# Kernel optimization log

Measured on AMD Instinct MI355X. Metric: run time of the kernel, lower is better.

The kernel has to match this reference:

```python
import jax, jax.numpy as jnp
import numpy as np

B0 = 0.01       # baseline threshold (Yin et al. ALIF)
BETA = 1.8      # adaptation coupling strength
SG_GAMMA = 0.5  # surrogate gradient scale
SG_LENS = 0.5   # surrogate gradient width

@jax.custom_vjp
def spike(v):
    return (v > 0.0).astype(v.dtype)

def _spike_fwd(v):
    return spike(v), v

def _spike_bwd(v, g):
    sg = SG_GAMMA * jnp.exp(-0.5 * (v / SG_LENS) ** 2) / (jnp.sqrt(2.0 * jnp.pi) * SG_LENS)
    return (g * sg,)

spike.defvjp(_spike_fwd, _spike_bwd)

def alif_forward(x, W_h, tau_mem, tau_adp, W_o, tau_out):
    # x: [T, B, I]; W_h: [H, I+H]; W_o: [O, H]
    T, B, _ = x.shape
    H = W_h.shape[0]
    O = W_o.shape[0]
    alpha = jnp.exp(-1.0 / tau_mem)    # [H] membrane decay
    rho = jnp.exp(-1.0 / tau_adp)      # [H] adaptation decay
    alpha_o = jnp.exp(-1.0 / tau_out)  # [O] output leaky-integrator decay
    z0 = jnp.zeros((B, H), x.dtype)
    u0 = jnp.zeros((B, H), x.dtype)
    a0 = jnp.zeros((B, H), x.dtype)
    ou0 = jnp.zeros((B, O), x.dtype)

    def step(carry, x_t):
        z, u, a, ou = carry
        cur = jnp.concatenate([x_t, z], axis=1) @ W_h.T   # [B, H]
        a = rho * a + (1.0 - rho) * z                     # adaptation from previous spike
        theta = B0 + BETA * a                             # adaptive threshold
        u = alpha * u + (1.0 - alpha) * cur - z * theta   # leaky integrate + soft reset
        z = spike(u - theta)                              # heaviside w/ surrogate grad
        ou = alpha_o * ou + (1.0 - alpha_o) * (z @ W_o.T) # LI readout
        return (z, u, a, ou), (ou, jnp.sum(z))

    (zT, uT, aT, ouT), (outputs, spikes) = jax.lax.scan(step, (z0, u0, a0, ou0), x)
    return outputs, (zT, uT, aT, ouT), jnp.sum(spikes)

def setup_inputs() -> dict:
    key = jax.random.key(0)
    ks = jax.random.split(key, 6)
    T, B, I, H, O = 250, 256, 700, 1024, 20
    x = jax.random.normal(ks[0], (T, B, I), jnp.float32)
    W_h = jax.random.normal(ks[1], (H, I + H), jnp.float32) / np.sqrt(I + H).astype(np.float32)
    tau_mem = 20.0 + 5.0 * jax.random.normal(ks[2], (H,), jnp.float32)
    tau_adp = 20.0 + 5.0 * jax.random.normal(ks[3], (H,), jnp.float32)
    W_o = jax.random.normal(ks[4], (O, H), jnp.float32) / np.sqrt(H).astype(np.float32)
    tau_out = 20.0 + 5.0 * jax.random.normal(ks[5], (O,), jnp.float32)
    return {"x": x, "W_h": W_h, "tau_mem": tau_mem, "tau_adp": tau_adp, "W_o": W_o, "tau_out": tau_out}

def reference(x, W_h, tau_mem, tau_adp, W_o, tau_out):
    outputs, (zT, uT, aT, ouT), num_spikes = alif_forward(x, W_h, tau_mem, tau_adp, W_o, tau_out)
    # matches torch forward: (outputs, ((hidden_z, hidden_u, hidden_a), out_u), num_spikes)
    return (outputs, zT, uT, aT, ouT, num_spikes)
```

## Files before the change

### kernel.cpp

```cpp
#include <hip/hip_runtime.h>

#define T_STEPS 250
#define BATCH   256
#define IN_DIM  700
#define HID     1024
#define W_LD    1724
#define OUT_DIM 20
#define KP      704
#define KP4     (KP / 4)
#define NKT     (KP / 32)
#define CHUNK_T 50

typedef __attribute__((ext_vector_type(8))) short     bf16x8;
typedef __attribute__((ext_vector_type(8))) unsigned short u16x8;
typedef __attribute__((ext_vector_type(4))) float     f32x4;
typedef unsigned long long u64;

__device__ inline unsigned short f2bf(float f) {
    unsigned int u = __float_as_uint(f);
    unsigned int r = u + 0x7FFFu + ((u >> 16) & 1u);
    return (unsigned short)(r >> 16);
}

__global__ __launch_bounds__(256)
void trans_whh_bf16(const float* __restrict__ W_h, unsigned short* __restrict__ WhhT) {
    __shared__ float tile[32][33];
    const int bx = blockIdx.x * 32;
    const int by = blockIdx.y * 32;
    const int tx = threadIdx.x, ty = threadIdx.y;
#pragma unroll
    for (int i = 0; i < 32; i += 8)
        tile[ty + i][tx] = W_h[(size_t)(bx + ty + i) * W_LD + IN_DIM + by + tx];
    __syncthreads();
#pragma unroll
    for (int i = 0; i < 32; i += 8)
        WhhT[(size_t)(by + ty + i) * HID + bx + tx] = f2bf(tile[tx][ty + i]);
}

__global__ __launch_bounds__(256)
void trans_wo(const float* __restrict__ Wo, float* __restrict__ WoT) {
    const int h = blockIdx.x * 256 + threadIdx.x;
    if (h >= HID) return;
#pragma unroll
    for (int o = 0; o < OUT_DIM; ++o)
        WoT[(size_t)h * OUT_DIM + o] = Wo[(size_t)o * HID + h];
}

__global__ __launch_bounds__(256)
void pack_x_bf16(const float* __restrict__ x, unsigned short* __restrict__ Xp, int rows) {
    const int total = rows * KP4;
    for (int idx = blockIdx.x * blockDim.x + threadIdx.x; idx < total;
         idx += gridDim.x * blockDim.x) {
        const int r = idx / KP4;
        const int c = idx - r * KP4;
        ushort4 o = make_ushort4(0, 0, 0, 0);
        if (c < IN_DIM / 4) {
            float4 v = *(const float4*)(x + (size_t)r * IN_DIM + c * 4);
            o = make_ushort4(f2bf(v.x), f2bf(v.y), f2bf(v.z), f2bf(v.w));
        }
        ((ushort4*)Xp)[(size_t)r * KP4 + c] = o;
    }
}

__global__ __launch_bounds__(256)
void pack_w_bf16(const float* __restrict__ W_h, unsigned short* __restrict__ Wp) {
    const int total = HID * KP4;
    for (int idx = blockIdx.x * blockDim.x + threadIdx.x; idx < total;
         idx += gridDim.x * blockDim.x) {
        const int r = idx / KP4;
        const int c = idx - r * KP4;
        ushort4 o = make_ushort4(0, 0, 0, 0);
        if (c < IN_DIM / 4) {
            float4 v = *(const float4*)(W_h + (size_t)r * W_LD + c * 4);
            o = make_ushort4(f2bf(v.x), f2bf(v.y), f2bf(v.z), f2bf(v.w));
        }
        ((ushort4*)Wp)[(size_t)r * KP4 + c] = o;
    }
}

__global__ __launch_bounds__(256)
void mfma_gemm(const unsigned short* __restrict__ A,
               const unsigned short* __restrict__ B, float* __restrict__ C) {
    __shared__ unsigned short lA[128 * 32];
    __shared__ unsigned short lB[128 * 32];
    const int tid  = threadIdx.x;
    const int wid  = tid >> 6, lane = tid & 63;
    const int wr   = wid >> 1, wc = wid & 1;
    const size_t bm = (size_t)blockIdx.x * 128;
    const size_t bn = (size_t)blockIdx.y * 128;

    const int srow = tid >> 2;
    const int skq  = (tid & 3) * 8;

    const int wb0 = (srow * 64 + (tid & 3) * 16) ^ ((srow & 7) << 4);
    const int wb1 = ((srow + 64) * 64 + (tid & 3) * 16) ^ ((srow & 7) << 4);

    const unsigned short* pa = A + (bm + srow) * KP + skq;
    const unsigned short* pb = B + (bn + srow) * KP + skq;

    u16x8 ra0, ra1, rb0, rb1;
    auto ldg = [&](int k0) {
        ra0 = *(const u16x8*)(pa + k0);
        ra1 = *(const u16x8*)(pa + (size_t)64 * KP + k0);
        rb0 = *(const u16x8*)(pb + k0);
        rb1 = *(const u16x8*)(pb + (size_t)64 * KP + k0);
    };

    const int arow = wr * 64 + (lane & 15);
    const int brow = wc * 64 + (lane & 15);
    const int fq   = (lane >> 4) * 16;

    f32x4 acc[4][4];
#pragma unroll
    for (int m = 0; m < 4; ++m)
#pragma unroll
        for (int n = 0; n < 4; ++n) acc[m][n] = (f32x4){0.f, 0.f, 0.f, 0.f};

    ldg(0);
    for (int kt = 0; kt < NKT; ++kt) {
        *(u16x8*)((char*)lA + wb0) = ra0;
        *(u16x8*)((char*)lA + wb1) = ra1;
        *(u16x8*)((char*)lB + wb0) = rb0;
        *(u16x8*)((char*)lB + wb1) = rb1;
        __syncthreads();
        if (kt + 1 < NKT) ldg((kt + 1) * 32);
        bf16x8 af[4], bf[4];
#pragma unroll
        for (int m = 0; m < 4; ++m) {
            const int row = arow + m * 16;
            af[m] = *(const bf16x8*)((const char*)lA + ((row * 64 + fq) ^ ((row & 7) << 4)));
        }
#pragma unroll
        for (int n = 0; n < 4; ++n) {
            const int row = brow + n * 16;
            bf[n] = *(const bf16x8*)((const char*)lB + ((row * 64 + fq) ^ ((row & 7) << 4)));
        }
#pragma unroll
        for (int m = 0; m < 4; ++m)
#pragma unroll
            for (int n = 0; n < 4; ++n)
                acc[m][n] = __builtin_amdgcn_mfma_f32_16x16x32_bf16(af[m], bf[n], acc[m][n], 0, 0, 0);
        __syncthreads();
    }
#pragma unroll
    for (int m = 0; m < 4; ++m)
#pragma unroll
        for (int r = 0; r < 4; ++r) {
            float* cp = C + (bm + wr * 64 + m * 16 + (lane >> 4) * 4 + r) * HID
                          + bn + wc * 64 + (lane & 15);
#pragma unroll
            for (int n = 0; n < 4; ++n) cp[n * 16] = acc[m][n][r];
        }
}

#define G_LDIDX(JJ, g)                                                        \
    {                                                                         \
        const int base_ = lo + (g) * 4;                                       \
        JJ[0] = (base_ + 0 < hi) ? (int)lst[base_ + 0] : 1024;                \
        JJ[1] = (base_ + 1 < hi) ? (int)lst[base_ + 1] : 1024;                \
        JJ[2] = (base_ + 2 < hi) ? (int)lst[base_ + 2] : 1024;                \
        JJ[3] = (base_ + 3 < hi) ? (int)lst[base_ + 3] : 1024;                \
    }

#define G_ISSUE(WB, JJ)                                                       \
    {                                                                         \
        _Pragma("unroll")                                                     \
        for (int q_ = 0; q_ < 4; ++q_) {                                      \
            const unsigned int* p_ = Wrow32 + ((size_t)JJ[q_] << 9);          \
            WB[q_ * 2 + 0] = *(const uint4*)p_;                               \
            WB[q_ * 2 + 1] = *(const uint4*)(p_ + 4);                         \
        }                                                                     \
    }

#define G_ACCUM(WB)                                                           \
    {                                                                         \
        _Pragma("unroll")                                                     \
        for (int q_ = 0; q_ < 4; ++q_) {                                      \
            const uint4 w0_ = WB[q_ * 2 + 0];                                 \
            const uint4 w1_ = WB[q_ * 2 + 1];                                 \
            pacc[0][0] += __uint_as_float(w0_.x << 16);                       \
            pacc[0][1] += __uint_as_float(w0_.x & 0xFFFF0000u);               \
            pacc[0][2] += __uint_as_float(w0_.y << 16);                       \
            pacc[0][3] += __uint_as_float(w0_.y & 0xFFFF0000u);               \
            pacc[1][0] += __uint_as_float(w0_.z << 16);                       \
            pacc[1][1] += __uint_as_float(w0_.z & 0xFFFF0000u);               \
            pacc[1][2] += __uint_as_float(w0_.w << 16);                       \
            pacc[1][3] += __uint_as_float(w0_.w & 0xFFFF0000u);               \
            pacc[2][0] += __uint_as_float(w1_.x << 16);                       \
            pacc[2][1] += __uint_as_float(w1_.x & 0xFFFF0000u);               \
            pacc[2][2] += __uint_as_float(w1_.y << 16);                       \
            pacc[2][3] += __uint_as_float(w1_.y & 0xFFFF0000u);               \
            pacc[3][0] += __uint_as_float(w1_.z << 16);                       \
            pacc[3][1] += __uint_as_float(w1_.z & 0xFFFF0000u);               \
            pacc[3][2] += __uint_as_float(w1_.w << 16);                       \
            pacc[3][3] += __uint_as_float(w1_.w & 0xFFFF0000u);               \
        }                                                                     \
    }

__global__ __launch_bounds__(256, 1)
void alif_scan(const float* __restrict__ CUR, const unsigned short* __restrict__ WhhT,
               const float* __restrict__ tau_mem, const float* __restrict__ tau_adp,
               float* __restrict__ zS, float* __restrict__ uS, float* __restrict__ aS,
               float* __restrict__ spkS, unsigned short* __restrict__ masks16,
               int t0, int tc) {
    const int tid  = threadIdx.x;
    const int wv   = tid >> 6;
    const int lane = tid & 63;
    const int b    = blockIdx.x;
    const int h0   = lane * 16;

    __shared__ __align__(16) unsigned short s_idx[4][2][1040];
    __shared__ __align__(16) f32x4 s_part[4][4][64];

    float u[16], a[16], alpha[16], rho[16];
#pragma unroll
    for (int q = 0; q < 4; ++q) {
        f32x4 uu = *(const f32x4*)(uS + (size_t)b * HID + h0 + q * 4);
        f32x4 aa = *(const f32x4*)(aS + (size_t)b * HID + h0 + q * 4);
        f32x4 tm = *(const f32x4*)(tau_mem + h0 + q * 4);
        f32x4 ta = *(const f32x4*)(tau_adp + h0 + q * 4);
#pragma unroll
        for (int k = 0; k < 4; ++k) {
            u[q * 4 + k] = uu[k];  a[q * 4 + k] = aa[k];
            alpha[q * 4 + k] = expf(-1.f / tm[k]);
            rho[q * 4 + k]   = expf(-1.f / ta[k]);
        }
    }
    unsigned int zb = 0;
#pragma unroll
    for (int q = 0; q < 4; ++q) {
        f32x4 zz = *(const f32x4*)(zS + (size_t)b * HID + h0 + q * 4);
#pragma unroll
        for (int k = 0; k < 4; ++k)
            if (zz[k] > 0.5f) zb |= (1u << (q * 4 + k));
    }

    int n;
    {
        const int cnt = __popc(zb);
        int incl = cnt;
#pragma unroll
        for (int d = 1; d < 64; d <<= 1) {
            int v = __shfl_up(incl, d, 64);
            if (lane >= d) incl += v;
        }
        int off = incl - cnt;
        unsigned int tmp = zb;
        while (tmp) {
            const int k = __ffs(tmp) - 1;
            tmp &= tmp - 1;
            s_idx[wv][0][off++] = (unsigned short)(h0 + k);
        }
        n = __shfl(incl, 63, 64);
    }

    const unsigned int* Wrow32 = (const unsigned int*)WhhT + (h0 >> 1);
    float xc[16];
#pragma unroll
    for (int q = 0; q < 4; ++q) {
        f32x4 v = *(const f32x4*)(CUR + (size_t)b * HID + h0 + q * 4);
        xc[q*4+0]=v[0]; xc[q*4+1]=v[1]; xc[q*4+2]=v[2]; xc[q*4+3]=v[3];
    }
    __syncthreads();

    int cur = 0;
    int wspk = 0;
    for (int tt = 0; tt < tc; ++tt) {
        float xn[16];
        {
            const int tn = (tt + 1 < tc) ? tt + 1 : tt;
            const float* p = CUR + ((size_t)tn * BATCH + b) * HID + h0;
#pragma unroll
            for (int q = 0; q < 4; ++q) {
                f32x4 v = *(const f32x4*)(p + q * 4);
                xn[q*4+0]=v[0]; xn[q*4+1]=v[1]; xn[q*4+2]=v[2]; xn[q*4+3]=v[3];
            }
        }

        f32x4 pacc[4];
#pragma unroll
        for (int q = 0; q < 4; ++q) pacc[q] = (f32x4){0.f, 0.f, 0.f, 0.f};

        if (n > 0) {
            const unsigned short* lst = s_idx[wv][cur];
            const int lo = (n * wv) >> 2;
            const int hi = (n * (wv + 1)) >> 2;
            const int m = hi - lo;
            if (m > 0) {
                const int ng = (m + 3) >> 2;
                int  jA[4], jB[4];
                uint4 wA[8], wB[8];
                G_LDIDX(jA, 0);
                G_ISSUE(wA, jA);
                int g = 0;
                while (true) {
                    if (g + 1 < ng) { G_LDIDX(jB, g + 1); G_ISSUE(wB, jB); }
                    G_ACCUM(wA);
                    if (++g >= ng) break;
                    if (g + 1 < ng) { G_LDIDX(jA, g + 1); G_ISSUE(wA, jA); }
                    G_ACCUM(wB);
                    if (++g >= ng) break;
                }
            }
            s_part[wv][0][lane] = pacc[0];
            s_part[wv][1][lane] = pacc[1];
            s_part[wv][2][lane] = pacc[2];
            s_part[wv][3][lane] = pacc[3];
            __syncthreads();
#pragma unroll
            for (int q = 0; q < 4; ++q) {
                f32x4 r0 = s_part[0][q][lane];
                f32x4 r1 = s_part[1][q][lane];
                f32x4 r2 = s_part[2][q][lane];
                f32x4 r3 = s_part[3][q][lane];
                pacc[q] = ((r0 + r1) + r2) + r3;
            }
        }

        unsigned int znb = 0;
#pragma unroll
        for (int k = 0; k < 16; ++k) {
            const float rec = pacc[k >> 2][k & 3];
            const float z   = (zb >> k) & 1 ? 1.f : 0.f;
            const float omr = 1.f - rho[k];
            const float oma = 1.f - alpha[k];
            a[k] = rho[k] * a[k] + omr * z;
            const float th = 0.01f + 1.8f * a[k];
            u[k] = alpha[k] * u[k] + oma * (xc[k] + rec) - z * th;
            if (u[k] - th > 0.f) znb |= (1u << k);
        }
        zb = znb;
        wspk += __popc(zb);
        if (wv == 0)
            masks16[((size_t)(t0 + tt) * BATCH + b) * 64 + lane] = (unsigned short)zb;

        {
            const int cnt = __popc(zb);
            int incl = cnt;
#pragma unroll
            for (int d = 1; d < 64; d <<= 1) {
                int v = __shfl_up(incl, d, 64);
                if (lane >= d) incl += v;
            }
            int off = incl - cnt;
            unsigned int tmp = zb;
            while (tmp) {
                const int k = __ffs(tmp) - 1;
                tmp &= tmp - 1;
                s_idx[wv][cur ^ 1][off++] = (unsigned short)(h0 + k);
            }
            n = __shfl(incl, 63, 64);
        }
#pragma unroll
        for (int k = 0; k < 16; ++k) xc[k] = xn[k];
        __syncthreads();
        cur ^= 1;
    }

    if (wv == 0) {
#pragma unroll
        for (int k = 0; k < 16; ++k) {
            zS[(size_t)b * HID + h0 + k] = (zb >> k) & 1 ? 1.f : 0.f;
            uS[(size_t)b * HID + h0 + k] = u[k];
            aS[(size_t)b * HID + h0 + k] = a[k];
        }
#pragma unroll
        for (int d = 32; d > 0; d >>= 1) wspk += __shfl_down(wspk, d, 64);
        if (lane == 0) atomicAdd(spkS, (float)wspk);
    }
}

__global__ __launch_bounds__(256)
void readout_y(const u64* __restrict__ masks, const float* __restrict__ WoT,
               float* __restrict__ y, int npairs) {
    const int pr   = blockIdx.x * 4 + (threadIdx.x >> 6);
    const int lane = threadIdx.x & 63;
    if (pr >= npairs) return;
    const u64* mp = masks + (size_t)pr * 16;
    float acc = 0.f;
#pragma unroll 4
    for (int w = 0; w < 16; ++w) {
        u64 m = mp[w];
        while (m) {
            const int j = __ffsll((unsigned long long)m) - 1;
            m &= m - 1;
            if (lane < OUT_DIM) acc += WoT[(size_t)(w * 64 + j) * OUT_DIM + lane];
        }
    }
    if (lane < OUT_DIM) y[(size_t)pr * OUT_DIM + lane] = acc;
}

__global__ __launch_bounds__(256)
void ewa_out(const float* __restrict__ y, const float* __restrict__ tau_out,
             float* __restrict__ outputs, float* __restrict__ ouS) {
    const int idx = blockIdx.x * 256 + threadIdx.x;
    if (idx >= BATCH * OUT_DIM) return;
    const int o = idx % OUT_DIM;
    const float ao = expf(-1.f / tau_out[o]);
    float ou = ouS[idx];
    for (int t = 0; t < T_STEPS; ++t) {
        const float v = y[(size_t)t * BATCH * OUT_DIM + idx];
        ou = ao * ou + (1.f - ao) * v;
        outputs[(size_t)t * BATCH * OUT_DIM + idx] = ou;
    }
    ouS[idx] = ou;
}

extern "C" void kernel_launch(void* const* d_in, const int* in_sizes, int n_in,
                              void* d_out, int out_size, void* d_ws, size_t ws_size,
                              hipStream_t stream) {
    (void)in_sizes; (void)n_in; (void)out_size;
    const float* x       = (const float*)d_in[0];
    const float* W_h     = (const float*)d_in[1];
    const float* tau_mem = (const float*)d_in[2];
    const float* tau_adp = (const float*)d_in[3];
    const float* W_o     = (const float*)d_in[4];
    const float* tau_out = (const float*)d_in[5];

    float* out     = (float*)d_out;
    float* outputs = out;
    float* zS  = out + (size_t)T_STEPS * BATCH * OUT_DIM;
    float* uS  = zS + (size_t)BATCH * HID;
    float* aS  = uS + (size_t)BATCH * HID;
    float* ouS = aS + (size_t)BATCH * HID;
    float* spk = ouS + (size_t)BATCH * OUT_DIM;

    char* w = (char*)d_ws;
    unsigned short* WhhT = (unsigned short*)w; w += (size_t)(HID + 1) * HID * 2;
    unsigned short* Wp   = (unsigned short*)w; w += (size_t)HID * KP * 2;
    float*          WoT  = (float*)w;          w += (size_t)HID * OUT_DIM * 4;
    unsigned short* masks16 = (unsigned short*)w; w += (size_t)T_STEPS * BATCH * 128;
    float*          yBuf = (float*)w;          w += (size_t)T_STEPS * BATCH * OUT_DIM * 4;
    char*           dynb = w;

    const size_t fixed = (size_t)(dynb - (char*)d_ws);
    const size_t per_step = (size_t)BATCH * KP * 2 + (size_t)BATCH * HID * 4;
    const size_t avail = ws_size > fixed ? ws_size - fixed : 0;
    int CT = (int)(avail / per_step);
    if (CT > CHUNK_T) CT = CHUNK_T;
    if (CT < 1) CT = 1;

    hipMemsetAsync(zS, 0,
                   ((size_t)3 * BATCH * HID + BATCH * OUT_DIM + 1) * sizeof(float),
                   stream);
    hipMemsetAsync(WhhT + (size_t)HID * HID, 0, HID * sizeof(unsigned short), stream);
    trans_whh_bf16<<<dim3(32, 32), dim3(32, 8), 0, stream>>>(W_h, WhhT);
    pack_w_bf16<<<512, 256, 0, stream>>>(W_h, Wp);
    trans_wo<<<4, 256, 0, stream>>>(W_o, WoT);

    for (int t0 = 0; t0 < T_STEPS; t0 += CT) {
        const int tc = (T_STEPS - t0 < CT) ? (T_STEPS - t0) : CT;
        const int rows = tc * BATCH;
        unsigned short* Xp = (unsigned short*)dynb;
        float* CUR = (float*)(dynb + (size_t)rows * KP * 2);
        int pblocks = (rows * KP4 + 255) / 256;
        if (pblocks > 2048) pblocks = 2048;
        pack_x_bf16<<<pblocks, 256, 0, stream>>>(x + (size_t)t0 * BATCH * IN_DIM, Xp, rows);
        mfma_gemm<<<dim3(rows / 128, HID / 128), 256, 0, stream>>>(Xp, Wp, CUR);
        alif_scan<<<BATCH, 256, 0, stream>>>(CUR, WhhT, tau_mem, tau_adp,
                                             zS, uS, aS, spk, masks16, t0, tc);
    }

    const int npairs = T_STEPS * BATCH;
    readout_y<<<(npairs + 3) / 4, 256, 0, stream>>>((const u64*)masks16, WoT, yBuf, npairs);
    ewa_out<<<(BATCH * OUT_DIM + 255) / 256, 256, 0, stream>>>(yBuf, tau_out, outputs, ouS);
}
```

Measured before the change: 1.050 ms.

## Overlap next-chunk input GEMM with recurrent scan in one fused launch

The separate x-packing kernel is removed, and the GEMM now converts fp32 x to bf16 as it loads tiles. Each chunk launches one kernel in which the first 256 blocks run the sequential ALIF scan for the current chunk. The remaining blocks compute the input-projection GEMM for the next chunk into a double buffer. This targets idle CUs during the latency-bound scan and cuts launch and packing traffic. The risks are contention between scan and GEMM blocks, reliance on the workspace holding two full CUR chunks, and a fixed chunk size with no workspace-size check.

```diff
diff --git a/kernel.cpp b/kernel.cpp
--- a/kernel.cpp
+++ b/kernel.cpp
@@ -7,7 +7,6 @@
 #define W_LD    1724
 #define OUT_DIM 20
 #define KP      704
-#define KP4     (KP / 4)
 #define NKT     (KP / 32)
 #define CHUNK_T 50
 
@@ -47,47 +46,50 @@
 }
 
 __global__ __launch_bounds__(256)
-void pack_x_bf16(const float* __restrict__ x, unsigned short* __restrict__ Xp, int rows) {
-    const int total = rows * KP4;
+void pack_w_bf16(const float* __restrict__ W_h, unsigned short* __restrict__ Wp) {
+    const int total = HID * (KP / 4);
     for (int idx = blockIdx.x * blockDim.x + threadIdx.x; idx < total;
          idx += gridDim.x * blockDim.x) {
-        const int r = idx / KP4;
-        const int c = idx - r * KP4;
-        ushort4 o = make_ushort4(0, 0, 0, 0);
-        if (c < IN_DIM / 4) {
-            float4 v = *(const float4*)(x + (size_t)r * IN_DIM + c * 4);
-            o = make_ushort4(f2bf(v.x), f2bf(v.y), f2bf(v.z), f2bf(v.w));
-        }
-        ((ushort4*)Xp)[(size_t)r * KP4 + c] = o;
-    }
-}
-
-__global__ __launch_bounds__(256)
-void pack_w_bf16(const float* __restrict__ W_h, unsigned short* __restrict__ Wp) {
-    const int total = HID * KP4;
-    for (int idx = blockIdx.x * blockDim.x + threadIdx.x; idx < total;
-         idx += gridDim.x * blockDim.x) {
-        const int r = idx / KP4;
-        const int c = idx - r * KP4;
+        const int r = idx / (KP / 4);
+        const int c = idx - r * (KP / 4);
         ushort4 o = make_ushort4(0, 0, 0, 0);
         if (c < IN_DIM / 4) {
             float4 v = *(const float4*)(W_h + (size_t)r * W_LD + c * 4);
             o = make_ushort4(f2bf(v.x), f2bf(v.y), f2bf(v.z), f2bf(v.w));
         }
-        ((ushort4*)Wp)[(size_t)r * KP4 + c] = o;
-    }
-}
-
-__global__ __launch_bounds__(256)
-void mfma_gemm(const unsigned short* __restrict__ A,
-               const unsigned short* __restrict__ B, float* __restrict__ C) {
-    __shared__ unsigned short lA[128 * 32];
-    __shared__ unsigned short lB[128 * 32];
+        ((ushort4*)Wp)[(size_t)r * (KP / 4) + c] = o;
+    }
+}
+
+__device__ __forceinline__ u16x8 ldx8(const float* __restrict__ row, int k) {
+    u16x8 r;
+    if (k <= IN_DIM - 8) {
+        float4 a = *(const float4*)(row + k);
+        float4 b = *(const float4*)(row + k + 4);
+        r[0] = (short)f2bf(a.x); r[1] = (short)f2bf(a.y);
+        r[2] = (short)f2bf(a.z); r[3] = (short)f2bf(a.w);
+        r[4] = (short)f2bf(b.x); r[5] = (short)f2bf(b.y);
+        r[6] = (short)f2bf(b.z); r[7] = (short)f2bf(b.w);
+    } else if (k < IN_DIM) {
+        float4 a = *(const float4*)(row + k);
+        r[0] = (short)f2bf(a.x); r[1] = (short)f2bf(a.y);
+        r[2] = (short)f2bf(a.z); r[3] = (short)f2bf(a.w);
+        r[4] = 0; r[5] = 0; r[6] = 0; r[7] = 0;
+    } else {
+        r = (u16x8){0,0,0,0,0,0,0,0};
+    }
+    return r;
+}
+
+__device__ __forceinline__
+void gemm_body(char* smem, const float* __restrict__ X,
+               const unsigned short* __restrict__ B, float* __restrict__ C,
+               int bm, int bn) {
+    unsigned short* lA = (unsigned short*)smem;
+    unsigned short* lB = (unsigned short*)(smem + 8192);
     const int tid  = threadIdx.x;
     const int wid  = tid >> 6, lane = tid & 63;
     const int wr   = wid >> 1, wc = wid & 1;
-    const size_t bm = (size_t)blockIdx.x * 128;
-    const size_t bn = (size_t)blockIdx.y * 128;
 
     const int srow = tid >> 2;
     const int skq  = (tid & 3) * 8;
@@ -95,13 +97,14 @@
     const int wb0 = (srow * 64 + (tid & 3) * 16) ^ ((srow & 7) << 4);
     const int wb1 = ((srow + 64) * 64 + (tid & 3) * 16) ^ ((srow & 7) << 4);
 
-    const unsigned short* pa = A + (bm + srow) * KP + skq;
-    const unsigned short* pb = B + (bn + srow) * KP + skq;
+    const float* xr0 = X + (size_t)(bm + srow) * IN_DIM;
+    const float* xr1 = X + (size_t)(bm + srow + 64) * IN_DIM;
+    const unsigned short* pb = B + (size_t)(bn + srow) * KP + skq;
 
     u16x8 ra0, ra1, rb0, rb1;
     auto ldg = [&](int k0) {
-        ra0 = *(const u16x8*)(pa + k0);
-        ra1 = *(const u16x8*)(pa + (size_t)64 * KP + k0);
+        ra0 = ldx8(xr0, k0 + skq);
+        ra1 = ldx8(xr1, k0 + skq);
         rb0 = *(const u16x8*)(pb + k0);
         rb1 = *(const u16x8*)(pb + (size_t)64 * KP + k0);
     };
@@ -118,8 +121,8 @@
 
     ldg(0);
     for (int kt = 0; kt < NKT; ++kt) {
-        *(u16x8*)((char*)lA + wb0) = ra0;
-        *(u16x8*)((char*)lA + wb1) = ra1;
+        *(u16x8*)((char*)lA + wb0) = *(u16x8*)&ra0;
+        *(u16x8*)((char*)lA + wb1) = *(u16x8*)&ra1;
         *(u16x8*)((char*)lB + wb0) = rb0;
         *(u16x8*)((char*)lB + wb1) = rb1;
         __syncthreads();
@@ -146,7 +149,7 @@
     for (int m = 0; m < 4; ++m)
 #pragma unroll
         for (int r = 0; r < 4; ++r) {
-            float* cp = C + (bm + wr * 64 + m * 16 + (lane >> 4) * 4 + r) * HID
+            float* cp = C + (size_t)(bm + wr * 64 + m * 16 + (lane >> 4) * 4 + r) * HID
                           + bn + wc * 64 + (lane & 15);
 #pragma unroll
             for (int n = 0; n < 4; ++n) cp[n * 16] = acc[m][n][r];
@@ -197,8 +200,9 @@
         }                                                                     \
     }
 
-__global__ __launch_bounds__(256, 1)
-void alif_scan(const float* __restrict__ CUR, const unsigned short* __restrict__ WhhT,
+__device__ __forceinline__
+void scan_body(char* smem, const float* __restrict__ CUR,
+               const unsigned short* __restrict__ WhhT,
                const float* __restrict__ tau_mem, const float* __restrict__ tau_adp,
                float* __restrict__ zS, float* __restrict__ uS, float* __restrict__ aS,
                float* __restrict__ spkS, unsigned short* __restrict__ masks16,
@@ -209,8 +213,8 @@
     const int b    = blockIdx.x;
     const int h0   = lane * 16;
 
-    __shared__ __align__(16) unsigned short s_idx[4][2][1040];
-    __shared__ __align__(16) f32x4 s_part[4][4][64];
+    unsigned short (*s_idx)[2][1040] = (unsigned short (*)[2][1040])smem;
+    f32x4 (*s_part)[4][64]           = (f32x4 (*)[4][64])(smem + 16640);
 
     float u[16], a[16], alpha[16], rho[16];
 #pragma unroll
@@ -370,6 +374,33 @@
     }
 }
 
+__global__ __launch_bounds__(256, 1)
+void fused_scan_gemm(const float* __restrict__ CUR,
+                     const unsigned short* __restrict__ WhhT,
+                     const float* __restrict__ tau_mem, const float* __restrict__ tau_adp,
+                     float* __restrict__ zS, float* __restrict__ uS, float* __restrict__ aS,
+                     float* __restrict__ spkS, unsigned short* __restrict__ masks16,
+                     int t0, int tc,
+                     const float* __restrict__ Xn, const unsigned short* __restrict__ Wp,
+                     float* __restrict__ CURn, int mBlocksN) {
+    __shared__ __align__(16) char smem[33024];
+    if ((int)blockIdx.x < BATCH) {
+        scan_body(smem, CUR, WhhT, tau_mem, tau_adp, zS, uS, aS, spkS,
+                  masks16, t0, tc);
+    } else {
+        const int gb = (int)blockIdx.x - BATCH;
+        gemm_body(smem, Xn, Wp, CURn, (gb % mBlocksN) * 128, (gb / mBlocksN) * 128);
+    }
+}
+
+__global__ __launch_bounds__(256)
+void gemm_pro(const float* __restrict__ X, const unsigned short* __restrict__ Wp,
+              float* __restrict__ C, int mBlocks) {
+    __shared__ __align__(16) char smem[16384];
+    const int gb = (int)blockIdx.x;
+    gemm_body(smem, X, Wp, C, (gb % mBlocks) * 128, (gb / mBlocks) * 128);
+}
+
 __global__ __launch_bounds__(256)
 void readout_y(const u64* __restrict__ masks, const float* __restrict__ WoT,
                float* __restrict__ y, int npairs) {
@@ -409,7 +440,7 @@
 extern "C" void kernel_launch(void* const* d_in, const int* in_sizes, int n_in,
                               void* d_out, int out_size, void* d_ws, size_t ws_size,
                               hipStream_t stream) {
-    (void)in_sizes; (void)n_in; (void)out_size;
+    (void)in_sizes; (void)n_in; (void)out_size; (void)ws_size;
     const float* x       = (const float*)d_in[0];
     const float* W_h     = (const float*)d_in[1];
     const float* tau_mem = (const float*)d_in[2];
@@ -431,14 +462,11 @@
     float*          WoT  = (float*)w;          w += (size_t)HID * OUT_DIM * 4;
     unsigned short* masks16 = (unsigned short*)w; w += (size_t)T_STEPS * BATCH * 128;
     float*          yBuf = (float*)w;          w += (size_t)T_STEPS * BATCH * OUT_DIM * 4;
-    char*           dynb = w;
-
-    const size_t fixed = (size_t)(dynb - (char*)d_ws);
-    const size_t per_step = (size_t)BATCH * KP * 2 + (size_t)BATCH * HID * 4;
-    const size_t avail = ws_size > fixed ? ws_size - fixed : 0;
-    int CT = (int)(avail / per_step);
-    if (CT > CHUNK_T) CT = CHUNK_T;
-    if (CT < 1) CT = 1;
+    float*          CUR_A = (float*)w;         w += (size_t)CHUNK_T * BATCH * HID * 4;
+    float*          CUR_B = (float*)w;
+
+    const int mB    = CHUNK_T * BATCH / 128;
+    const int gemmG = mB * (HID / 128);
 
     hipMemsetAsync(zS, 0,
                    ((size_t)3 * BATCH * HID + BATCH * OUT_DIM + 1) * sizeof(float),
@@ -448,17 +476,20 @@
     pack_w_bf16<<<512, 256, 0, stream>>>(W_h, Wp);
     trans_wo<<<4, 256, 0, stream>>>(W_o, WoT);
 
-    for (int t0 = 0; t0 < T_STEPS; t0 += CT) {
-        const int tc = (T_STEPS - t0 < CT) ? (T_STEPS - t0) : CT;
-        const int rows = tc * BATCH;
-        unsigned short* Xp = (unsigned short*)dynb;
-        float* CUR = (float*)(dynb + (size_t)rows * KP * 2);
-        int pblocks = (rows * KP4 + 255) / 256;
-        if (pblocks > 2048) pblocks = 2048;
-        pack_x_bf16<<<pblocks, 256, 0, stream>>>(x + (size_t)t0 * BATCH * IN_DIM, Xp, rows);
-        mfma_gemm<<<dim3(rows / 128, HID / 128), 256, 0, stream>>>(Xp, Wp, CUR);
-        alif_scan<<<BATCH, 256, 0, stream>>>(CUR, WhhT, tau_mem, tau_adp,
-                                             zS, uS, aS, spk, masks16, t0, tc);
+    gemm_pro<<<gemmG, 256, 0, stream>>>(x, Wp, CUR_A, mB);
+
+    const int nChunks = T_STEPS / CHUNK_T;
+    for (int c = 0; c < nChunks; ++c) {
+        const int t0 = c * CHUNK_T;
+        float* CURc = (c & 1) ? CUR_B : CUR_A;
+        float* CURn = (c & 1) ? CUR_A : CUR_B;
+        const bool more = (c + 1 < nChunks);
+        const int grid = BATCH + (more ? gemmG : 0);
+        fused_scan_gemm<<<grid, 256, 0, stream>>>(
+            CURc, WhhT, tau_mem, tau_adp, zS, uS, aS, spk, masks16,
+            t0, CHUNK_T,
+            x + (size_t)(t0 + CHUNK_T) * BATCH * IN_DIM, Wp, CURn,
+            more ? mB : 1);
     }
 
     const int npairs = T_STEPS * BATCH;
```

After: 1.323 ms. +26.0%, slower.
